# Kernel tuning notes

Hardware: AMD Instinct MI355X
Metric: run time of the kernel (lower is better)

The kernel has to match this reference:

```python
import jax, jax.numpy as jnp
import numpy as np

N = 100000
E = 1600000
IN_FEATS = 256
OUT_FEATS = 128
THRESHOLD = 0.5


def setup_inputs() -> dict:
    key = jax.random.key(0)
    k1, k2, k3, k4, k5, k6, k7 = jax.random.split(key, 7)
    return {
        "feat": jax.random.normal(k1, (N, IN_FEATS), dtype=jnp.float32),
        "src": jax.random.randint(k2, (E,), 0, N, dtype=jnp.int32),
        "dst": jax.random.randint(k3, (E,), 0, N, dtype=jnp.int32),
        "edge_weight": jax.random.uniform(k4, (E,), dtype=jnp.float32),
        "weight": jax.random.normal(k5, (IN_FEATS, OUT_FEATS), dtype=jnp.float32),
        "bias": jax.random.normal(k6, (OUT_FEATS,), dtype=jnp.float32),
        "mask_real": jax.random.uniform(k7, (IN_FEATS, OUT_FEATS), dtype=jnp.float32),
    }


def reference(feat, src, dst, edge_weight, weight, bias, mask_real):
    ones_e = jnp.ones((E,), dtype=feat.dtype)
    # norm == 'both': scale source feats by out_degree^-0.5 (clamped at 1)
    out_deg = jnp.clip(jax.ops.segment_sum(ones_e, src, num_segments=N), 1.0)
    feat_src = feat * (out_deg ** -0.5)[:, None]  # [N, IN]
    # binarized mask with straight-through estimator (training-mode path)
    hard = (mask_real > THRESHOLD).astype(mask_real.dtype)
    mask_t = jax.lax.stop_gradient(hard - mask_real) + mask_real
    w = mask_t * weight  # [IN, OUT]
    # in_feats > out_feats: project before aggregation
    feat_src = feat_src @ w  # [N, OUT]
    # u_mul_e then sum: gather source feats, scale by edge weight, scatter-add to dst
    msgs = feat_src[src] * edge_weight[:, None]  # [E, OUT]
    rst = jax.ops.segment_sum(msgs, dst, num_segments=N)  # [N, OUT]
    # norm == 'both': scale by in_degree^-0.5 (clamped at 1)
    in_deg = jnp.clip(jax.ops.segment_sum(ones_e, dst, num_segments=N), 1.0)
    rst = rst * (in_deg ** -0.5)[:, None]
    return rst + bias
```

## Files before the change

### kernel.cpp

```cpp
#include <hip/hip_runtime.h>

#define N_NODES 100000
#define N_EDGES 1600000
#define IN_F 256
#define OUT_F 128
#define NBUCK 391
#define NPART 256
#define CHUNK (N_EDGES / NPART)
#define BCAP 5632

#define ODBLK 256
#define ODCHUNK (N_EDGES / ODBLK)
#define ODW 25000

typedef __attribute__((ext_vector_type(8))) short short8;
typedef __attribute__((ext_vector_type(4))) float f32x4;

__device__ __forceinline__ unsigned bf16_rne(float f) {
    unsigned u = __float_as_uint(f);
    return (u + 0x7fffu + ((u >> 16) & 1u)) >> 16;
}

__global__ void mask_w_kernel(const float* __restrict__ weight,
                              const float* __restrict__ mask_real,
                              unsigned short* __restrict__ wmT) {
    int i = blockIdx.x * blockDim.x + threadIdx.x;
    if (i < IN_F * OUT_F) {
        int k = i >> 7;
        int n = i & 127;
        float v = (mask_real[i] > 0.5f) ? weight[i] : 0.0f;
        wmT[(size_t)n * IN_F + k] = (unsigned short)bf16_rne(v);
    }
}

__global__ __launch_bounds__(256) void outdeg_part_kernel(const int* __restrict__ src,
                                                          unsigned* __restrict__ part) {
    __shared__ unsigned h[ODW];
    int b = blockIdx.x, t = threadIdx.x;
    for (int i = t; i < ODW; i += 256) h[i] = 0u;
    __syncthreads();
    int base = b * ODCHUNK;
    for (int i = t; i < ODCHUNK; i += 256) {
        unsigned s = (unsigned)src[base + i];
        atomicAdd(&h[s >> 2], 1u << ((s & 3u) * 8u));
    }
    __syncthreads();
    unsigned* op = part + (size_t)b * ODW;
    for (int i = t; i < ODW; i += 256) op[i] = h[i];
}

__global__ __launch_bounds__(256) void outdeg_reduce_kernel(const unsigned* __restrict__ part,
                                                            unsigned* __restrict__ outpk) {
    int d = blockIdx.x * 256 + threadIdx.x;
    if (d < ODW) {
        unsigned sum = 0u;
#pragma unroll 8
        for (int b = 0; b < ODBLK; b++) sum += part[(size_t)b * ODW + d];
        outpk[d] = sum;
    }
}

__global__ __launch_bounds__(256) void hist_kernel(const int* __restrict__ dst,
                                                   unsigned* __restrict__ hist) {
    __shared__ unsigned h[NBUCK];
    int p = blockIdx.x, t = threadIdx.x;
    for (int b = t; b < NBUCK; b += 256) h[b] = 0u;
    __syncthreads();
    int base = p * CHUNK;
    for (int i = t; i < CHUNK; i += 256)
        atomicAdd(&h[(unsigned)dst[base + i] >> 8], 1u);
    __syncthreads();
    for (int b = t; b < NBUCK; b += 256)
        hist[(size_t)p * NBUCK + b] = h[b];
}

__global__ __launch_bounds__(256) void scan_reduce_hist(const unsigned* __restrict__ hist,
                                                        unsigned* __restrict__ bsum) {
    __shared__ unsigned red[256];
    int b = blockIdx.x, t = threadIdx.x;
    red[t] = hist[(size_t)t * NBUCK + b];
    __syncthreads();
#pragma unroll
    for (int d = 128; d > 0; d >>= 1) {
        if (t < d) red[t] += red[t + d];
        __syncthreads();
    }
    if (t == 0) bsum[b] = red[0];
}

__global__ __launch_bounds__(512) void scan_spine(const unsigned* __restrict__ bsum,
                                                  unsigned* __restrict__ bpref) {
    __shared__ unsigned part[512];
    int t = threadIdx.x;
    unsigned v = (t < NBUCK) ? bsum[t] : 0u;
    part[t] = v;
    __syncthreads();
#pragma unroll
    for (int d = 1; d < 512; d <<= 1) {
        unsigned x = (t >= d) ? part[t - d] : 0u;
        __syncthreads();
        part[t] += x;
        __syncthreads();
    }
    if (t < NBUCK) bpref[t] = part[t] - v;
}

__global__ __launch_bounds__(256) void scan_apply_hist(const unsigned* __restrict__ hist,
                                                       const unsigned* __restrict__ bpref,
                                                       unsigned* __restrict__ scanned) {
    __shared__ unsigned part[256];
    int b = blockIdx.x, t = threadIdx.x;
    unsigned v = hist[(size_t)t * NBUCK + b];
    part[t] = v;
    __syncthreads();
#pragma unroll
    for (int d = 1; d < 256; d <<= 1) {
        unsigned x = (t >= d) ? part[t - d] : 0u;
        __syncthreads();
        part[t] += x;
        __syncthreads();
    }
    scanned[(size_t)b * 256 + t] = bpref[b] + part[t] - v;
}

__global__ __launch_bounds__(256) void scatter_kernel(const int* __restrict__ src,
                                                      const int* __restrict__ dst,
                                                      const float* __restrict__ ew,
                                                      const unsigned* __restrict__ scanned,
                                                      uint2* __restrict__ tmp) {
    __shared__ unsigned cur[NBUCK];
    int p = blockIdx.x, t = threadIdx.x;
    for (int b = t; b < NBUCK; b += 256) cur[b] = scanned[(size_t)b * 256 + p];
    __syncthreads();
    int base = p * CHUNK;
    for (int i = t; i < CHUNK; i += 256) {
        int e = base + i;
        int s = src[e];
        int d = dst[e];
        unsigned pos = atomicAdd(&cur[(unsigned)d >> 8], 1u);
        tmp[pos] = make_uint2((unsigned)s | (((unsigned)d & 255u) << 17),
                              __float_as_uint(ew[e]));
    }
}

__global__ __launch_bounds__(256) void fillB_kernel(const uint2* __restrict__ tmp,
                                                    const unsigned* __restrict__ scanned,
                                                    unsigned* __restrict__ offsets,
                                                    unsigned* __restrict__ smeta) {
    __shared__ uint2 ebuf[BCAP];
    __shared__ unsigned hcnt[256];
    __shared__ unsigned pref[256];
    int b = blockIdx.x, t = threadIdx.x;
    unsigned base = scanned[(size_t)b * 256];
    unsigned next = (b == NBUCK - 1) ? (unsigned)N_EDGES : scanned[(size_t)(b + 1) * 256];
    int cnt = (int)(next - base);
    if (cnt > BCAP) cnt = BCAP;
    hcnt[t] = 0u;
    for (int i = t; i < cnt; i += 256) ebuf[i] = tmp[base + i];
    __syncthreads();
    for (int i = t; i < cnt; i += 256) atomicAdd(&hcnt[ebuf[i].x >> 17], 1u);
    __syncthreads();
    unsigned v = hcnt[t];
    pref[t] = v;
    __syncthreads();
#pragma unroll
    for (int d = 1; d < 256; d <<= 1) {
        unsigned x = (t >= d) ? pref[t - d] : 0u;
        __syncthreads();
        pref[t] += x;
        __syncthreads();
    }
    unsigned excl = pref[t] - v;
    int node = b * 256 + t;
    if (node <= N_NODES) offsets[node] = base + excl;
    hcnt[t] = base + excl;
    __syncthreads();
    for (int i = t; i < cnt; i += 256) {
        uint2 m = ebuf[i];
        unsigned pos = atomicAdd(&hcnt[m.x >> 17], 1u);
        smeta[pos] = ((m.y + 0x10000u) & 0xFFFE0000u) | (m.x & 0x1FFFFu);
    }
}

__global__ __launch_bounds__(256) void gemm_kernel(const float* __restrict__ feat,
                                                   const unsigned short* __restrict__ wmT,
                                                   const unsigned char* __restrict__ outdeg8,
                                                   unsigned short* __restrict__ hb) {
    __shared__ unsigned short sB[128][264];
    int t = threadIdx.x;
    for (int idx = t; idx < (128 * 256 / 8); idx += 256) {
        int flat = idx * 8;
        int n = flat >> 8, k = flat & 255;
        *(uint4*)&sB[n][k] = *(const uint4*)&wmT[flat];
    }
    __syncthreads();

    int lane = t & 63, wv = t >> 6;
    int m16 = lane & 15, quad = lane >> 4;
    int row0 = blockIdx.x * 64;
    int arow = min(row0 + wv * 16 + m16, N_NODES - 1);
    const float* fp = feat + (size_t)arow * IN_F + quad * 8;

    f32x4 acc[8];
#pragma unroll
    for (int i = 0; i < 8; i++) acc[i] = (f32x4){0.f, 0.f, 0.f, 0.f};

#pragma unroll
    for (int k0 = 0; k0 < IN_F; k0 += 32) {
        float4 v0 = *(const float4*)(fp + k0);
        float4 v1 = *(const float4*)(fp + k0 + 4);
        uint4 pk;
        pk.x = bf16_rne(v0.x) | (bf16_rne(v0.y) << 16);
        pk.y = bf16_rne(v0.z) | (bf16_rne(v0.w) << 16);
        pk.z = bf16_rne(v1.x) | (bf16_rne(v1.y) << 16);
        pk.w = bf16_rne(v1.z) | (bf16_rne(v1.w) << 16);
        short8 a;
        *(uint4*)&a = pk;
#pragma unroll
        for (int nt = 0; nt < 8; nt++) {
            short8 b = *(const short8*)&sB[nt * 16 + m16][k0 + quad * 8];
            acc[nt] = __builtin_amdgcn_mfma_f32_16x16x32_bf16(a, b, acc[nt], 0, 0, 0);
        }
    }
#pragma unroll
    for (int reg = 0; reg < 4; reg++) {
        int row = row0 + wv * 16 + quad * 4 + reg;
        if (row < N_NODES) {
            float s = rsqrtf(fmaxf((float)outdeg8[row], 1.0f));
#pragma unroll
            for (int nt = 0; nt < 8; nt++)
                hb[(size_t)row * OUT_F + nt * 16 + m16] =
                    (unsigned short)bf16_rne(acc[nt][reg] * s);
        }
    }
}

__global__ __launch_bounds__(256) void gather_kernel(const unsigned* __restrict__ smeta,
                                                     const unsigned* __restrict__ offsets,
                                                     const uint4* __restrict__ hrows4,
                                                     const float* __restrict__ bias,
                                                     float* __restrict__ out) {
    int lane = threadIdx.x & 63;
    int n = blockIdx.x * 4 + (threadIdx.x >> 6);
    int g = lane >> 4;
    int q = lane & 15;
    unsigned beg = offsets[n], end = offsets[n + 1];
    int deg = (int)(end - beg);

    float acc[8];
#pragma unroll
    for (int i = 0; i < 8; i++) acc[i] = 0.0f;

    for (int base = 0; base < deg; base += 64) {
        int c = min(64, deg - base);
        unsigned pv = 0u;
        if (lane < c) pv = smeta[beg + base + lane];
        int nch = (c + 3) >> 2;
#pragma unroll 4
        for (int j = 0; j < nch; j++) {
            int ei = (j << 2) + g;
            unsigned p = __shfl(pv, ei);
            unsigned s = p & 0x1FFFFu;
            float w = __uint_as_float(p & 0xFFFE0000u);
            uint4 h = hrows4[(size_t)s * 16u + q];
            acc[0] = fmaf(__uint_as_float(h.x << 16), w, acc[0]);
            acc[1] = fmaf(__uint_as_float(h.x & 0xffff0000u), w, acc[1]);
            acc[2] = fmaf(__uint_as_float(h.y << 16), w, acc[2]);
            acc[3] = fmaf(__uint_as_float(h.y & 0xffff0000u), w, acc[3]);
            acc[4] = fmaf(__uint_as_float(h.z << 16), w, acc[4]);
            acc[5] = fmaf(__uint_as_float(h.z & 0xffff0000u), w, acc[5]);
            acc[6] = fmaf(__uint_as_float(h.w << 16), w, acc[6]);
            acc[7] = fmaf(__uint_as_float(h.w & 0xffff0000u), w, acc[7]);
        }
    }

#pragma unroll
    for (int i = 0; i < 8; i++) {
        acc[i] += __shfl_xor(acc[i], 16);
        acc[i] += __shfl_xor(acc[i], 32);
    }

    float o0, o1;
    if (g == 0)      { o0 = acc[0]; o1 = acc[1]; }
    else if (g == 1) { o0 = acc[2]; o1 = acc[3]; }
    else if (g == 2) { o0 = acc[4]; o1 = acc[5]; }
    else             { o0 = acc[6]; o1 = acc[7]; }

    float sc = rsqrtf(fmaxf((float)deg, 1.0f));
    int col = q * 8 + g * 2;
    float2 b = *(const float2*)&bias[col];
    float2 o = make_float2(o0 * sc + b.x, o1 * sc + b.y);
    *(float2*)&out[(size_t)n * OUT_F + col] = o;
}

extern "C" void kernel_launch(void* const* d_in, const int* in_sizes, int n_in,
                              void* d_out, int out_size, void* d_ws, size_t ws_size,
                              hipStream_t stream) {
    const float* feat      = (const float*)d_in[0];
    const int*   src       = (const int*)d_in[1];
    const int*   dst       = (const int*)d_in[2];
    const float* ew        = (const float*)d_in[3];
    const float* weight    = (const float*)d_in[4];
    const float* bias      = (const float*)d_in[5];
    const float* mask_real = (const float*)d_in[6];
    float* out = (float*)d_out;

    char* ws = (char*)d_ws;
    size_t o = 0;
    auto take = [&](size_t bytes) {
        char* p = ws + o;
        o = (o + bytes + 255) & ~(size_t)255;
        return p;
    };
    unsigned short* wmT     = (unsigned short*)take((size_t)IN_F * OUT_F * 2);
    unsigned*       outpk   = (unsigned*)take((size_t)ODW * 4);
    unsigned*       offs    = (unsigned*)take((size_t)(N_NODES + 1) * 4);
    unsigned*       hist    = (unsigned*)take((size_t)NPART * NBUCK * 4);
    unsigned*       scanned = (unsigned*)take((size_t)NBUCK * 256 * 4);
    unsigned*       bsum    = (unsigned*)take((size_t)NBUCK * 4);
    unsigned*       bpref   = (unsigned*)take((size_t)NBUCK * 4);
    uint2*          tmp     = (uint2*)take((size_t)N_EDGES * 8);
    unsigned*       smeta   = (unsigned*)take((size_t)N_EDGES * 4);
    unsigned short* hrows   = (unsigned short*)take((size_t)N_NODES * OUT_F * 2);

    unsigned* odpart = (unsigned*)tmp;

    mask_w_kernel<<<(IN_F * OUT_F + 255) / 256, 256, 0, stream>>>(weight, mask_real, wmT);
    outdeg_part_kernel<<<ODBLK, 256, 0, stream>>>(src, odpart);
    outdeg_reduce_kernel<<<(ODW + 255) / 256, 256, 0, stream>>>(odpart, outpk);
    hist_kernel<<<NPART, 256, 0, stream>>>(dst, hist);
    scan_reduce_hist<<<NBUCK, 256, 0, stream>>>(hist, bsum);
    scan_spine<<<1, 512, 0, stream>>>(bsum, bpref);
    scan_apply_hist<<<NBUCK, 256, 0, stream>>>(hist, bpref, scanned);
    scatter_kernel<<<NPART, 256, 0, stream>>>(src, dst, ew, scanned, tmp);
    gemm_kernel<<<(N_NODES + 63) / 64, 256, 0, stream>>>(feat, wmT,
                                                         (const unsigned char*)outpk, hrows);
    fillB_kernel<<<NBUCK, 256, 0, stream>>>(tmp, scanned, offs, smeta);
    gather_kernel<<<N_NODES / 4, 256, 0, stream>>>(smeta, offs,
                                                   (const uint4*)hrows, bias, out);
}
```

Measured before the change: 358.5 us.

## Fuse preprocessing kernels and hoist GEMM feature loads ahead of MFMA loop

Merges the mask-weight, out-degree partial histogram and dst bucket histogram kernels into one launch. The out-degree reduction and bucket-sum reduction now share a second launch, and the spine scan is folded into the scan-apply kernel, which recomputes each bucket prefix by summing earlier bucket totals. This cuts the launch count from seven preprocessing kernels to three and reads src/dst once together. Separately, the GEMM now issues all 16 float4 feature loads up front before the MFMA loop, which raises register pressure in exchange for more memory-level parallelism.

```diff
diff --git a/kernel.cpp b/kernel.cpp
--- a/kernel.cpp
+++ b/kernel.cpp
@@ -9,9 +9,8 @@
 #define CHUNK (N_EDGES / NPART)
 #define BCAP 5632
 
-#define ODBLK 256
-#define ODCHUNK (N_EDGES / ODBLK)
 #define ODW 25000
+#define ODRB ((ODW + 255) / 256)
 
 typedef __attribute__((ext_vector_type(8))) short short8;
 typedef __attribute__((ext_vector_type(4))) float f32x4;
@@ -21,95 +20,81 @@
     return (u + 0x7fffu + ((u >> 16) & 1u)) >> 16;
 }
 
-__global__ void mask_w_kernel(const float* __restrict__ weight,
-                              const float* __restrict__ mask_real,
-                              unsigned short* __restrict__ wmT) {
-    int i = blockIdx.x * blockDim.x + threadIdx.x;
-    if (i < IN_F * OUT_F) {
-        int k = i >> 7;
-        int n = i & 127;
+__global__ __launch_bounds__(256) void fused_pre_kernel(const int* __restrict__ src,
+                                                        const int* __restrict__ dst,
+                                                        const float* __restrict__ weight,
+                                                        const float* __restrict__ mask_real,
+                                                        unsigned* __restrict__ part,
+                                                        unsigned* __restrict__ hist,
+                                                        unsigned short* __restrict__ wmT) {
+    __shared__ unsigned h[ODW];
+    __shared__ unsigned hh[NBUCK];
+    int b = blockIdx.x, t = threadIdx.x;
+    for (int i = t; i < ODW; i += 256) h[i] = 0u;
+    for (int i = t; i < NBUCK; i += 256) hh[i] = 0u;
+    if (t < 128) {
+        int i = b * 128 + t;
+        int k = i >> 7, n = i & 127;
         float v = (mask_real[i] > 0.5f) ? weight[i] : 0.0f;
         wmT[(size_t)n * IN_F + k] = (unsigned short)bf16_rne(v);
     }
-}
-
-__global__ __launch_bounds__(256) void outdeg_part_kernel(const int* __restrict__ src,
-                                                          unsigned* __restrict__ part) {
-    __shared__ unsigned h[ODW];
-    int b = blockIdx.x, t = threadIdx.x;
-    for (int i = t; i < ODW; i += 256) h[i] = 0u;
-    __syncthreads();
-    int base = b * ODCHUNK;
-    for (int i = t; i < ODCHUNK; i += 256) {
+    __syncthreads();
+    int base = b * CHUNK;
+    for (int i = t; i < CHUNK; i += 256) {
         unsigned s = (unsigned)src[base + i];
+        unsigned d = (unsigned)dst[base + i];
         atomicAdd(&h[s >> 2], 1u << ((s & 3u) * 8u));
+        atomicAdd(&hh[d >> 8], 1u);
     }
     __syncthreads();
     unsigned* op = part + (size_t)b * ODW;
     for (int i = t; i < ODW; i += 256) op[i] = h[i];
-}
-
-__global__ __launch_bounds__(256) void outdeg_reduce_kernel(const unsigned* __restrict__ part,
-                                                            unsigned* __restrict__ outpk) {
-    int d = blockIdx.x * 256 + threadIdx.x;
-    if (d < ODW) {
-        unsigned sum = 0u;
+    for (int i = t; i < NBUCK; i += 256) hist[(size_t)b * NBUCK + i] = hh[i];
+}
+
+__global__ __launch_bounds__(256) void fused_reduce_kernel(const unsigned* __restrict__ part,
+                                                           const unsigned* __restrict__ hist,
+                                                           unsigned* __restrict__ outpk,
+                                                           unsigned* __restrict__ bsum) {
+    int t = threadIdx.x;
+    if (blockIdx.x < ODRB) {
+        int d = blockIdx.x * 256 + t;
+        if (d < ODW) {
+            unsigned sum = 0u;
 #pragma unroll 8
-        for (int b = 0; b < ODBLK; b++) sum += part[(size_t)b * ODW + d];
-        outpk[d] = sum;
-    }
-}
-
-__global__ __launch_bounds__(256) void hist_kernel(const int* __restrict__ dst,
-                                                   unsigned* __restrict__ hist) {
-    __shared__ unsigned h[NBUCK];
-    int p = blockIdx.x, t = threadIdx.x;
-    for (int b = t; b < NBUCK; b += 256) h[b] = 0u;
-    __syncthreads();
-    int base = p * CHUNK;
-    for (int i = t; i < CHUNK; i += 256)
-        atomicAdd(&h[(unsigned)dst[base + i] >> 8], 1u);
-    __syncthreads();
-    for (int b = t; b < NBUCK; b += 256)
-        hist[(size_t)p * NBUCK + b] = h[b];
-}
-
-__global__ __launch_bounds__(256) void scan_reduce_hist(const unsigned* __restrict__ hist,
-                                                        unsigned* __restrict__ bsum) {
+            for (int b = 0; b < NPART; b++) sum += part[(size_t)b * ODW + d];
+            outpk[d] = sum;
+        }
+    } else {
+        __shared__ unsigned red[256];
+        int b = blockIdx.x - ODRB;
+        red[t] = hist[(size_t)t * NBUCK + b];
+        __syncthreads();
+#pragma unroll
+        for (int d = 128; d > 0; d >>= 1) {
+            if (t < d) red[t] += red[t + d];
+            __syncthreads();
+        }
+        if (t == 0) bsum[b] = red[0];
+    }
+}
+
+__global__ __launch_bounds__(256) void scan_apply_kernel(const unsigned* __restrict__ hist,
+                                                         const unsigned* __restrict__ bsum,
+                                                         unsigned* __restrict__ scanned) {
     __shared__ unsigned red[256];
+    __shared__ unsigned part[256];
     int b = blockIdx.x, t = threadIdx.x;
-    red[t] = hist[(size_t)t * NBUCK + b];
+    unsigned loc = 0u;
+    for (int i = t; i < b; i += 256) loc += bsum[i];
+    red[t] = loc;
     __syncthreads();
 #pragma unroll
     for (int d = 128; d > 0; d >>= 1) {
         if (t < d) red[t] += red[t + d];
         __syncthreads();
     }
-    if (t == 0) bsum[b] = red[0];
-}
-
-__global__ __launch_bounds__(512) void scan_spine(const unsigned* __restrict__ bsum,
-                                                  unsigned* __restrict__ bpref) {
-    __shared__ unsigned part[512];
-    int t = threadIdx.x;
-    unsigned v = (t < NBUCK) ? bsum[t] : 0u;
-    part[t] = v;
-    __syncthreads();
-#pragma unroll
-    for (int d = 1; d < 512; d <<= 1) {
-        unsigned x = (t >= d) ? part[t - d] : 0u;
-        __syncthreads();
-        part[t] += x;
-        __syncthreads();
-    }
-    if (t < NBUCK) bpref[t] = part[t] - v;
-}
-
-__global__ __launch_bounds__(256) void scan_apply_hist(const unsigned* __restrict__ hist,
-                                                       const unsigned* __restrict__ bpref,
-                                                       unsigned* __restrict__ scanned) {
-    __shared__ unsigned part[256];
-    int b = blockIdx.x, t = threadIdx.x;
+    unsigned bpref = red[0];
     unsigned v = hist[(size_t)t * NBUCK + b];
     part[t] = v;
     __syncthreads();
@@ -120,7 +105,7 @@
         part[t] += x;
         __syncthreads();
     }
-    scanned[(size_t)b * 256 + t] = bpref[b] + part[t] - v;
+    scanned[(size_t)b * 256 + t] = bpref + part[t] - v;
 }
 
 __global__ __launch_bounds__(256) void scatter_kernel(const int* __restrict__ src,
@@ -190,8 +175,7 @@
     int t = threadIdx.x;
     for (int idx = t; idx < (128 * 256 / 8); idx += 256) {
         int flat = idx * 8;
-        int n = flat >> 8, k = flat & 255;
-        *(uint4*)&sB[n][k] = *(const uint4*)&wmT[flat];
+        *(uint4*)&sB[flat >> 8][flat & 255] = *(const uint4*)&wmT[flat];
     }
     __syncthreads();
 
@@ -201,24 +185,29 @@
     int arow = min(row0 + wv * 16 + m16, N_NODES - 1);
     const float* fp = feat + (size_t)arow * IN_F + quad * 8;
 
+    float4 va[16];
+#pragma unroll
+    for (int i = 0; i < 8; i++) {
+        va[2 * i]     = *(const float4*)(fp + i * 32);
+        va[2 * i + 1] = *(const float4*)(fp + i * 32 + 4);
+    }
+
     f32x4 acc[8];
 #pragma unroll
     for (int i = 0; i < 8; i++) acc[i] = (f32x4){0.f, 0.f, 0.f, 0.f};
 
 #pragma unroll
-    for (int k0 = 0; k0 < IN_F; k0 += 32) {
-        float4 v0 = *(const float4*)(fp + k0);
-        float4 v1 = *(const float4*)(fp + k0 + 4);
+    for (int i = 0; i < 8; i++) {
         uint4 pk;
-        pk.x = bf16_rne(v0.x) | (bf16_rne(v0.y) << 16);
-        pk.y = bf16_rne(v0.z) | (bf16_rne(v0.w) << 16);
-        pk.z = bf16_rne(v1.x) | (bf16_rne(v1.y) << 16);
-        pk.w = bf16_rne(v1.z) | (bf16_rne(v1.w) << 16);
+        pk.x = bf16_rne(va[2 * i].x) | (bf16_rne(va[2 * i].y) << 16);
+        pk.y = bf16_rne(va[2 * i].z) | (bf16_rne(va[2 * i].w) << 16);
+        pk.z = bf16_rne(va[2 * i + 1].x) | (bf16_rne(va[2 * i + 1].y) << 16);
+        pk.w = bf16_rne(va[2 * i + 1].z) | (bf16_rne(va[2 * i + 1].w) << 16);
         short8 a;
         *(uint4*)&a = pk;
 #pragma unroll
         for (int nt = 0; nt < 8; nt++) {
-            short8 b = *(const short8*)&sB[nt * 16 + m16][k0 + quad * 8];
+            short8 b = *(const short8*)&sB[nt * 16 + m16][i * 32 + quad * 8];
             acc[nt] = __builtin_amdgcn_mfma_f32_16x16x32_bf16(a, b, acc[nt], 0, 0, 0);
         }
     }
@@ -318,20 +307,16 @@
     unsigned*       hist    = (unsigned*)take((size_t)NPART * NBUCK * 4);
     unsigned*       scanned = (unsigned*)take((size_t)NBUCK * 256 * 4);
     unsigned*       bsum    = (unsigned*)take((size_t)NBUCK * 4);
-    unsigned*       bpref   = (unsigned*)take((size_t)NBUCK * 4);
     uint2*          tmp     = (uint2*)take((size_t)N_EDGES * 8);
     unsigned*       smeta   = (unsigned*)take((size_t)N_EDGES * 4);
     unsigned short* hrows   = (unsigned short*)take((size_t)N_NODES * OUT_F * 2);
 
     unsigned* odpart = (unsigned*)tmp;
 
-    mask_w_kernel<<<(IN_F * OUT_F + 255) / 256, 256, 0, stream>>>(weight, mask_real, wmT);
-    outdeg_part_kernel<<<ODBLK, 256, 0, stream>>>(src, odpart);
-    outdeg_reduce_kernel<<<(ODW + 255) / 256, 256, 0, stream>>>(odpart, outpk);
-    hist_kernel<<<NPART, 256, 0, stream>>>(dst, hist);
-    scan_reduce_hist<<<NBUCK, 256, 0, stream>>>(hist, bsum);
-    scan_spine<<<1, 512, 0, stream>>>(bsum, bpref);
-    scan_apply_hist<<<NBUCK, 256, 0, stream>>>(hist, bpref, scanned);
+    fused_pre_kernel<<<NPART, 256, 0, stream>>>(src, dst, weight, mask_real,
+                                                odpart, hist, wmT);
+    fused_reduce_kernel<<<ODRB + NBUCK, 256, 0, stream>>>(odpart, hist, outpk, bsum);
+    scan_apply_kernel<<<NBUCK, 256, 0, stream>>>(hist, bsum, scanned);
     scatter_kernel<<<NPART, 256, 0, stream>>>(src, dst, ew, scanned, tmp);
     gemm_kernel<<<(N_NODES + 63) / 64, 256, 0, stream>>>(feat, wmT,
                                                          (const unsigned char*)outpk, hrows);
```

Measured after the change: 342.6 us. -4.4%, faster.
